# Kernel optimization log

Hardware: AMD Instinct MI355X
Metric: run time of the kernel (lower is better)

## Reference

```python
import math
import jax, jax.numpy as jnp
import numpy as np

H = 16          # n_heads
WIN = 512       # window_size (causal, one-sided)
BS = 64         # block_size


def setup_inputs() -> dict:
    key = jax.random.key(0)
    ks = jax.random.split(key, 5)
    B, T, D = 2, 4096, 1024
    x = jax.random.normal(ks[0], (B, T, D), dtype=jnp.float32)
    init = 0.02
    Wq = jax.random.normal(ks[1], (D, D), dtype=jnp.float32) * init
    Wk = jax.random.normal(ks[2], (D, D), dtype=jnp.float32) * init
    Wv = jax.random.normal(ks[3], (D, D), dtype=jnp.float32) * init
    Wo = jax.random.normal(ks[4], (D, D), dtype=jnp.float32) * init
    return {"x": x, "Wq": Wq, "Wk": Wk, "Wv": Wv, "Wo": Wo}


def _sliding_window_attn(q, k, v):
    """Causal sliding-window attention, banded/block-sparse form.

    q,k,v: (B, H, T, hd). Only key blocks within the window of each query
    block are gathered, honoring the sparsity the torch mask encodes.
    """
    B, Hn, T, hd = q.shape
    nb = T // BS                   # number of blocks
    nw1 = WIN // BS + 1            # key blocks touching a query block
    scale = 1.0 / math.sqrt(hd)

    qb = q.reshape(B, Hn, nb, BS, hd)
    kb = k.reshape(B, Hn, nb, BS, hd)
    vb = v.reshape(B, Hn, nb, BS, hd)

    offs = jnp.arange(-(WIN // BS), 1)                 # (nw1,)
    idx_raw = jnp.arange(nb)[:, None] + offs[None, :]  # (nb, nw1)
    idx = jnp.clip(idx_raw, 0, nb - 1)

    kg = jnp.take(kb, idx, axis=2)   # (B,H,nb,nw1,BS,hd)
    vg = jnp.take(vb, idx, axis=2)

    scores = jnp.einsum('bhnqd,bhnwkd->bhnqwk', qb, kg) * scale

    qpos = (jnp.arange(nb) * BS)[:, None, None, None] + jnp.arange(BS)[None, :, None, None]  # (nb,BS,1,1)
    kpos = (idx_raw * BS)[:, None, :, None] + jnp.arange(BS)[None, None, None, :]            # (nb,1,nw1,BS)
    valid = (idx_raw[:, None, :, None] >= 0) & (kpos <= qpos) & (qpos - kpos < WIN)
    scores = jnp.where(valid[None, None], scores, -1e9)

    p = jax.nn.softmax(scores.reshape(B, Hn, nb, BS, nw1 * BS), axis=-1)
    p = p.reshape(B, Hn, nb, BS, nw1, BS)
    out = jnp.einsum('bhnqwk,bhnwkd->bhnqd', p, vg)
    return out.reshape(B, Hn, T, hd)


def reference(x, Wq, Wk, Wv, Wo):
    B, T, D = x.shape
    hd = D // H

    def proj(W):  # torch Linear: x @ W.T
        return (x @ W.T).reshape(B, T, H, hd).transpose(0, 2, 1, 3)

    q, k, v = proj(Wq), proj(Wk), proj(Wv)
    out = _sliding_window_attn(q, k, v)            # (B,H,T,hd)
    out = out.transpose(0, 2, 1, 3).reshape(B, T, D)
    return out @ Wo.T
```

## Files before the change

### kernel.cpp

```cpp
#include <hip/hip_runtime.h>

#define DI static __device__ __forceinline__

typedef __attribute__((ext_vector_type(8))) short short8;
typedef __attribute__((ext_vector_type(4))) float f32x4;

DI unsigned short f2bf(float f) {
    union { float f; unsigned int u; } v; v.f = f;
    unsigned int r = v.u + 0x7FFFu + ((v.u >> 16) & 1u);
    return (unsigned short)(r >> 16);
}

DI unsigned int f2bf2(float lo, float hi) {
    return (unsigned int)f2bf(lo) | ((unsigned int)f2bf(hi) << 16);
}

DI void gload_lds16(const void* g, void* l) {
    __builtin_amdgcn_global_load_lds(
        (const __attribute__((address_space(1))) void*)g,
        (__attribute__((address_space(3))) void*)l, 16, 0, 0);
}

DI short8 ldsfrag(const void* base, int row, int bytecol) {
    return *(const short8*)((const char*)base + row * 128 + (bytecol ^ ((row & 7) << 4)));
}

__global__ __launch_bounds__(256) void k_cvt(
    const float* __restrict__ x, const float* __restrict__ wq,
    const float* __restrict__ wk, const float* __restrict__ wv,
    const float* __restrict__ wo,
    unsigned short* __restrict__ xb, unsigned short* __restrict__ wqb,
    unsigned short* __restrict__ wkb, unsigned short* __restrict__ wvb,
    unsigned short* __restrict__ wob)
{
    int idx = (blockIdx.x * 256 + threadIdx.x) * 8;
    const float* src; unsigned short* dst; int off;
    if (idx < 8388608) {
        src = x; dst = xb; off = idx;
    } else {
        int rel = idx - 8388608;
        int sel = rel >> 20;
        off = rel & 1048575;
        switch (sel) {
            case 0:  src = wq; dst = wqb; break;
            case 1:  src = wk; dst = wkb; break;
            case 2:  src = wv; dst = wvb; break;
            default: src = wo; dst = wob; break;
        }
    }
    float4 v0 = *(const float4*)(src + off);
    float4 v1 = *(const float4*)(src + off + 4);
    uint4 o;
    o.x = f2bf2(v0.x, v0.y);
    o.y = f2bf2(v0.z, v0.w);
    o.z = f2bf2(v1.x, v1.y);
    o.w = f2bf2(v1.z, v1.w);
    *(uint4*)(dst + off) = o;
}

DI void gemm_core(const unsigned short* __restrict__ Ag,
                  const unsigned short* __restrict__ Bg,
                  int m0, int n0, char* smem, f32x4 acc[4][4])
{
    const int t = threadIdx.x, lane = t & 63;
    const int wid = t >> 6, wr = wid >> 2, wc = wid & 3;
    const int kl = lane & 15, hi = lane >> 4;

#pragma unroll
    for (int m = 0; m < 4; ++m)
#pragma unroll
        for (int n = 0; n < 4; ++n)
            acc[m][n] = f32x4{0.f, 0.f, 0.f, 0.f};

    const int ca  = t,       ra  = ca  >> 2, sa  = ((ca  & 3) ^ ((ra  >> 1) & 3)) * 8;
    const int cb0 = t,       rb0 = cb0 >> 2, sb0 = ((cb0 & 3) ^ ((rb0 >> 1) & 3)) * 8;
    const int cb1 = t + 512, rb1 = cb1 >> 2, sb1 = ((cb1 & 3) ^ ((rb1 >> 1) & 3)) * 8;
    const unsigned short* pa  = Ag + (long)(m0 + ra)  * 1024 + sa;
    const unsigned short* pb0 = Bg + (long)(n0 + rb0) * 1024 + sb0;
    const unsigned short* pb1 = Bg + (long)(n0 + rb1) * 1024 + sb1;

#define STAGE(TILE, BUF) do {                                          \
        char* _sb = smem + (BUF) * 24576;                              \
        gload_lds16(pa  + (TILE) * 32, _sb + ca * 16);                 \
        gload_lds16(pb0 + (TILE) * 32, _sb + 8192 + cb0 * 16);         \
        gload_lds16(pb1 + (TILE) * 32, _sb + 8192 + cb1 * 16);         \
    } while (0)

    STAGE(0, 0);
    STAGE(1, 1);

    const int swz = ((hi ^ ((kl >> 1) & 3)) << 4);
    const int aoff = (wr * 64 + kl) * 64 + swz;
    const int boff = 8192 + (wc * 64 + kl) * 64 + swz;

#define KSTEP(KS, CUR, PRE, ISSUE, VM) do {                                   \
        asm volatile("s_waitcnt vmcnt(" VM ")" ::: "memory");                 \
        __builtin_amdgcn_s_barrier();                                         \
        __builtin_amdgcn_sched_barrier(0);                                    \
        if (ISSUE) STAGE((KS) + 2, PRE);                                      \
        const char* _ab = smem + (CUR) * 24576 + aoff;                        \
        const char* _bb = smem + (CUR) * 24576 + boff;                        \
        short8 _fa[4], _fb[4];                                                \
        _Pragma("unroll")                                                     \
        for (int m = 0; m < 4; ++m) _fa[m] = *(const short8*)(_ab + m * 1024);\
        _Pragma("unroll")                                                     \
        for (int n = 0; n < 4; ++n) _fb[n] = *(const short8*)(_bb + n * 1024);\
        __builtin_amdgcn_s_setprio(1);                                        \
        _Pragma("unroll")                                                     \
        for (int m = 0; m < 4; ++m)                                           \
        _Pragma("unroll")                                                     \
            for (int n = 0; n < 4; ++n)                                       \
                acc[m][n] = __builtin_amdgcn_mfma_f32_16x16x32_bf16(          \
                    _fa[m], _fb[n], acc[m][n], 0, 0, 0);                      \
        __builtin_amdgcn_s_setprio(0);                                        \
    } while (0)

    for (int u = 0; u < 10; ++u) {
        const int ks = u * 3;
        KSTEP(ks + 0, 0, 2, 1, "3");
        KSTEP(ks + 1, 1, 0, 1, "3");
        KSTEP(ks + 2, 2, 1, 1, "3");
    }
    KSTEP(30, 0, 2, 0, "3");
    KSTEP(31, 1, 0, 0, "0");
#undef KSTEP
#undef STAGE
}

DI void gemm_core128(const unsigned short* __restrict__ Ag,
                     const unsigned short* __restrict__ Bg,
                     int m0, int n0, char* smem, f32x4 acc[4][4])
{
    const int t = threadIdx.x, lane = t & 63;
    const int wid = t >> 6, wr = wid >> 1, wc = wid & 1;
    const int kl = lane & 15, hi = lane >> 4;

#pragma unroll
    for (int m = 0; m < 4; ++m)
#pragma unroll
        for (int n = 0; n < 4; ++n)
            acc[m][n] = f32x4{0.f, 0.f, 0.f, 0.f};

    const int ca0 = t,       ra0 = ca0 >> 2, sa0 = ((ca0 & 3) ^ ((ra0 >> 1) & 3)) * 8;
    const int ca1 = t + 256, ra1 = ca1 >> 2, sa1 = ((ca1 & 3) ^ ((ra1 >> 1) & 3)) * 8;
    const unsigned short* pa0 = Ag + (long)(m0 + ra0) * 1024 + sa0;
    const unsigned short* pa1 = Ag + (long)(m0 + ra1) * 1024 + sa1;
    const unsigned short* pb0 = Bg + (long)(n0 + ra0) * 1024 + sa0;
    const unsigned short* pb1 = Bg + (long)(n0 + ra1) * 1024 + sa1;

#define STAGE(TILE, BUF) do {                                          \
        char* _sb = smem + (BUF) * 16384;                              \
        gload_lds16(pa0 + (TILE) * 32, _sb + ca0 * 16);                \
        gload_lds16(pa1 + (TILE) * 32, _sb + ca1 * 16);                \
        gload_lds16(pb0 + (TILE) * 32, _sb + 8192 + ca0 * 16);         \
        gload_lds16(pb1 + (TILE) * 32, _sb + 8192 + ca1 * 16);         \
    } while (0)

    STAGE(0, 0);
    STAGE(1, 1);

    const int swz = ((hi ^ ((kl >> 1) & 3)) << 4);
    const int aoff = (wr * 64 + kl) * 64 + swz;
    const int boff = 8192 + (wc * 64 + kl) * 64 + swz;

#define KSTEP(KS, CUR, PRE, ISSUE, VM) do {                                   \
        asm volatile("s_waitcnt vmcnt(" VM ")" ::: "memory");                 \
        __builtin_amdgcn_s_barrier();                                         \
        __builtin_amdgcn_sched_barrier(0);                                    \
        if (ISSUE) STAGE((KS) + 2, PRE);                                      \
        const char* _ab = smem + (CUR) * 16384 + aoff;                        \
        const char* _bb = smem + (CUR) * 16384 + boff;                        \
        short8 _fa[4], _fb[4];                                                \
        _Pragma("unroll")                                                     \
        for (int m = 0; m < 4; ++m) _fa[m] = *(const short8*)(_ab + m * 1024);\
        _Pragma("unroll")                                                     \
        for (int n = 0; n < 4; ++n) _fb[n] = *(const short8*)(_bb + n * 1024);\
        __builtin_amdgcn_s_setprio(1);                                        \
        _Pragma("unroll")                                                     \
        for (int m = 0; m < 4; ++m)                                           \
        _Pragma("unroll")                                                     \
            for (int n = 0; n < 4; ++n)                                       \
                acc[m][n] = __builtin_amdgcn_mfma_f32_16x16x32_bf16(          \
                    _fa[m], _fb[n], acc[m][n], 0, 0, 0);                      \
        __builtin_amdgcn_s_setprio(0);                                        \
    } while (0)

    for (int u = 0; u < 10; ++u) {
        const int ks = u * 3;
        KSTEP(ks + 0, 0, 2, 1, "4");
        KSTEP(ks + 1, 1, 0, 1, "4");
        KSTEP(ks + 2, 2, 1, 1, "4");
    }
    KSTEP(30, 0, 2, 0, "4");
    KSTEP(31, 1, 0, 0, "0");
#undef KSTEP
#undef STAGE
}

__global__ __launch_bounds__(512, 4) void k_gemm_qkv(
    const unsigned short* __restrict__ xb,
    const unsigned short* __restrict__ wqb, const unsigned short* __restrict__ wkb,
    const unsigned short* __restrict__ wvb,
    unsigned short* __restrict__ Qo, unsigned short* __restrict__ Ko,
    unsigned short* __restrict__ VTo)
{
    extern __shared__ char smem[];
    const int bx = blockIdx.x, by = blockIdx.y;
    const int w = by >> 2, nb = by & 3;
    const unsigned short* Bw = (w == 0) ? wqb : ((w == 1) ? wkb : wvb);
    const float sc = (w == 0) ? 0.18033688011112042f : 1.0f;

    f32x4 acc[4][4];
    gemm_core(xb, Bw, bx * 128, nb * 256, smem, acc);

    const int t = threadIdx.x, lane = t & 63, wid = t >> 6;
    const int wr = wid >> 2, wc = wid & 3, kl = lane & 15, hi = lane >> 4;
    const int h = nb * 4 + wc;

    if (w < 2) {
        unsigned short* Ow = (w == 0) ? Qo : Ko;
#pragma unroll
        for (int m = 0; m < 4; ++m)
#pragma unroll
            for (int r = 0; r < 4; ++r) {
                int grow = bx * 128 + wr * 64 + m * 16 + hi * 4 + r;
                int bi = grow >> 12, tt = grow & 4095;
                unsigned short* rowp = Ow + ((long)(bi * 16 + h) * 4096 + tt) * 64;
#pragma unroll
                for (int n = 0; n < 4; ++n)
                    rowp[n * 16 + kl] = f2bf(acc[m][n][r] * sc);
            }
    } else {
#pragma unroll
        for (int m = 0; m < 4; ++m)
#pragma unroll
            for (int r = 0; r < 4; ++r) {
                int grow = bx * 128 + wr * 64 + m * 16 + hi * 4 + r;
                int bi = grow >> 12, tt = grow & 4095;
                unsigned short* hb = VTo + (long)(bi * 16 + h) * 262144;
#pragma unroll
                for (int n = 0; n < 4; ++n) {
                    int d = n * 16 + kl;
                    hb[(long)d * 4096 + tt] = f2bf(acc[m][n][r]);
                }
            }
    }
}

__global__ __launch_bounds__(512) void k_attn(
    const unsigned short* __restrict__ Q, const unsigned short* __restrict__ K,
    const unsigned short* __restrict__ VT, unsigned short* __restrict__ AO)
{
    __shared__ unsigned short Qs[8192];
    __shared__ unsigned short Ks[2][4096], Vs[2][4096];
    const int t = threadIdx.x, lane = t & 63, wid = t >> 6;
    const int kl = lane & 15, hi = lane >> 4;
    const int bid = blockIdx.x;
    const int sid = (bid & 7) * 128 + (bid >> 3);
    const int qi = sid & 31, bh = sid >> 5;
    const int b = bh >> 4, h = bh & 15;
    const int iA = qi * 2, iB = qi * 2 + 1;
    const int myI = (wid < 4) ? iA : iB;
    const char* qg = (const char*)(Q + ((long)bh * 4096 + qi * 128) * 64);
    const char* kg = (const char*)(K + (long)bh * 4096 * 64);
    const char* vg = (const char*)(VT + (long)bh * 64 * 4096);

    const int cq0 = t, cq1 = t + 512;
    const int rq0 = cq0 >> 3, sq0 = ((cq0 & 7) * 16) ^ ((rq0 & 7) << 4);
    const int rq1 = cq1 >> 3, sq1 = ((cq1 & 7) * 16) ^ ((rq1 & 7) << 4);
    const int rk = t >> 3, swk = ((t & 7) * 16) ^ ((rk & 7) << 4);
    const char* kgt = kg + rk * 128 + swk;
    const char* vgt = vg + rk * 8192 + swk;

    const int jlo = (iA >= 8) ? iA - 8 : 0;
    const int jhi = iB;

    gload_lds16(qg + rq0 * 128 + sq0, (char*)Qs + cq0 * 16);
    gload_lds16(qg + rq1 * 128 + sq1, (char*)Qs + cq1 * 16);
    gload_lds16(kgt + jlo * 8192, (char*)Ks[0] + t * 16);
    gload_lds16(vgt + jlo * 128,  (char*)Vs[0] + t * 16);
    __syncthreads();

    short8 aq[2];
    aq[0] = ldsfrag(Qs, wid * 16 + kl, hi * 16);
    aq[1] = ldsfrag(Qs, wid * 16 + kl, 64 + hi * 16);

    float lsum[4] = {0.f, 0.f, 0.f, 0.f};
    f32x4 o[4];
#pragma unroll
    for (int nt = 0; nt < 4; ++nt) o[nt] = f32x4{0.f, 0.f, 0.f, 0.f};

    const int qrow = (wid & 3) * 16 + hi * 4;
    char* pw = (char*)Qs + wid * 2048;

    for (int j = jlo; j <= jhi; ++j) {
        const int buf = (j - jlo) & 1;
        if (j < jhi) {
            const int nb = buf ^ 1;
            gload_lds16(kgt + (j + 1) * 8192, (char*)Ks[nb] + t * 16);
            gload_lds16(vgt + (j + 1) * 128,  (char*)Vs[nb] + t * 16);
        }

        const bool act = (wid < 4) ? (j <= iA) : (j >= iB - 8);
        if (act) {
            f32x4 s[4];
#pragma unroll
            for (int nt = 0; nt < 4; ++nt) {
                s[nt] = f32x4{0.f, 0.f, 0.f, 0.f};
#pragma unroll
                for (int kk = 0; kk < 2; ++kk)
                    s[nt] = __builtin_amdgcn_mfma_f32_16x16x32_bf16(
                        aq[kk], ldsfrag(Ks[buf], nt * 16 + kl, kk * 64 + hi * 16),
                        s[nt], 0, 0, 0);
            }

            if (j == myI) {
#pragma unroll
                for (int nt = 0; nt < 4; ++nt) {
                    int key = nt * 16 + kl;
#pragma unroll
                    for (int r = 0; r < 4; ++r)
                        if (key > qrow + r) s[nt][r] = -1e9f;
                }
            } else if (myI - j == 8) {
#pragma unroll
                for (int nt = 0; nt < 4; ++nt) {
                    int key = nt * 16 + kl;
#pragma unroll
                    for (int r = 0; r < 4; ++r)
                        if (key <= qrow + r) s[nt][r] = -1e9f;
                }
            }

#pragma unroll
            for (int nt = 0; nt < 4; ++nt)
#pragma unroll
                for (int r = 0; r < 4; ++r) {
                    float p = exp2f(s[nt][r]);
                    s[nt][r] = p;
                    lsum[r] += p;
                }

#pragma unroll
            for (int nt = 0; nt < 4; ++nt)
#pragma unroll
                for (int r = 0; r < 4; ++r) {
                    int q = hi * 4 + r;
                    int colb = (nt * 16 + kl) * 2;
                    *(unsigned short*)(pw + q * 128 + (colb ^ ((q & 7) << 4))) =
                        f2bf(s[nt][r]);
                }

            short8 pa0 = ldsfrag(pw, kl, hi * 16);
            short8 pa1 = ldsfrag(pw, kl, 64 + hi * 16);
#pragma unroll
            for (int nt = 0; nt < 4; ++nt) {
                o[nt] = __builtin_amdgcn_mfma_f32_16x16x32_bf16(
                    pa0, ldsfrag(Vs[buf], nt * 16 + kl, hi * 16), o[nt], 0, 0, 0);
                o[nt] = __builtin_amdgcn_mfma_f32_16x16x32_bf16(
                    pa1, ldsfrag(Vs[buf], nt * 16 + kl, 64 + hi * 16), o[nt], 0, 0, 0);
            }
        }

        __syncthreads();
    }

#pragma unroll
    for (int d = 1; d < 16; d <<= 1)
#pragma unroll
        for (int r = 0; r < 4; ++r) lsum[r] += __shfl_xor(lsum[r], d);

    float inv[4];
#pragma unroll
    for (int r = 0; r < 4; ++r) inv[r] = 1.0f / lsum[r];
#pragma unroll
    for (int r = 0; r < 4; ++r) {
        int tt = qi * 128 + wid * 16 + hi * 4 + r;
        unsigned short* rowp = AO + ((long)(b * 4096 + tt)) * 1024 + h * 64;
#pragma unroll
        for (int nt = 0; nt < 4; ++nt)
            rowp[nt * 16 + kl] = f2bf(o[nt][r] * inv[r]);
    }
}

__global__ __launch_bounds__(256, 3) void k_gemm_out(
    const unsigned short* __restrict__ AO, const unsigned short* __restrict__ wob,
    float* __restrict__ out)
{
    extern __shared__ char smem[];
    const int bx = blockIdx.x, nb = blockIdx.y;
    f32x4 acc[4][4];
    gemm_core128(AO, wob, bx * 128, nb * 128, smem, acc);

    const int t = threadIdx.x, lane = t & 63, wid = t >> 6;
    const int wr = wid >> 1, wc = wid & 1, kl = lane & 15, hi = lane >> 4;
#pragma unroll
    for (int m = 0; m < 4; ++m)
#pragma unroll
        for (int r = 0; r < 4; ++r) {
            int grow = bx * 128 + wr * 64 + m * 16 + hi * 4 + r;
            float* rowp = out + (long)grow * 1024 + nb * 128 + wc * 64;
#pragma unroll
            for (int n = 0; n < 4; ++n)
                rowp[n * 16 + kl] = acc[m][n][r];
        }
}

extern "C" void kernel_launch(void* const* d_in, const int* in_sizes, int n_in,
                              void* d_out, int out_size, void* d_ws, size_t ws_size,
                              hipStream_t stream) {
    const float* x  = (const float*)d_in[0];
    const float* wq = (const float*)d_in[1];
    const float* wk = (const float*)d_in[2];
    const float* wv = (const float*)d_in[3];
    const float* wo = (const float*)d_in[4];

    char* ws = (char*)d_ws;
    const size_t MB = 1024 * 1024;
    unsigned short* xb  = (unsigned short*)(ws);
    unsigned short* wqb = (unsigned short*)(ws + 16 * MB);
    unsigned short* wkb = (unsigned short*)(ws + 18 * MB);
    unsigned short* wvb = (unsigned short*)(ws + 20 * MB);
    unsigned short* wob = (unsigned short*)(ws + 22 * MB);
    unsigned short* Qp  = (unsigned short*)(ws + 24 * MB);
    unsigned short* Kp  = (unsigned short*)(ws + 40 * MB);
    unsigned short* VTp = (unsigned short*)(ws + 56 * MB);
    unsigned short* AOp = xb;

    hipFuncSetAttribute((const void*)k_gemm_qkv,
                        hipFuncAttributeMaxDynamicSharedMemorySize, 73728);
    hipFuncSetAttribute((const void*)k_gemm_out,
                        hipFuncAttributeMaxDynamicSharedMemorySize, 49152);

    dim3 blk(256);
    k_cvt<<<6144, blk, 0, stream>>>(x, wq, wk, wv, wo,
                                    xb, wqb, wkb, wvb, wob);
    k_gemm_qkv<<<dim3(64, 12), 512, 73728, stream>>>(xb, wqb, wkb, wvb,
                                                     Qp, Kp, VTp);
    k_attn<<<1024, 512, 0, stream>>>(Qp, Kp, VTp, AOp);
    k_gemm_out<<<dim3(64, 8), 256, 49152, stream>>>(AOp, wob, (float*)d_out);
}
```

Baseline: 135.6 us.

## Enlarge attention tile to 256 query rows, two sub-tiles per wave

Each attention block now covers four 64-row query blocks (256 rows) instead of two, and each wave handles 32 query rows as two 16-row sub-tiles. Every K/V block staged in LDS is therefore reused by more queries, so less K/V traffic and fewer synchronisations are needed per query. Q fragments are now loaded straight from global memory into registers instead of being staged through LDS. The trade-off is half as many workgroups (512), a longer serial key loop of up to 12 blocks, more accumulator registers per wave, and waves sitting idle at more iterations because of the window band.

```diff
diff --git a/kernel.cpp b/kernel.cpp
--- a/kernel.cpp
+++ b/kernel.cpp
@@ -251,47 +251,47 @@
     const unsigned short* __restrict__ Q, const unsigned short* __restrict__ K,
     const unsigned short* __restrict__ VT, unsigned short* __restrict__ AO)
 {
-    __shared__ unsigned short Qs[8192];
+    __shared__ unsigned short Ps[8192];
     __shared__ unsigned short Ks[2][4096], Vs[2][4096];
     const int t = threadIdx.x, lane = t & 63, wid = t >> 6;
     const int kl = lane & 15, hi = lane >> 4;
     const int bid = blockIdx.x;
-    const int sid = (bid & 7) * 128 + (bid >> 3);
-    const int qi = sid & 31, bh = sid >> 5;
+    const int sid = (bid & 7) * 64 + (bid >> 3);
+    const int qi = sid & 15, bh = sid >> 4;
     const int b = bh >> 4, h = bh & 15;
-    const int iA = qi * 2, iB = qi * 2 + 1;
-    const int myI = (wid < 4) ? iA : iB;
-    const char* qg = (const char*)(Q + ((long)bh * 4096 + qi * 128) * 64);
+    const int myI = qi * 4 + (wid >> 1);
+    const int rbase = (wid >> 1) * 64 + (wid & 1) * 32;
     const char* kg = (const char*)(K + (long)bh * 4096 * 64);
     const char* vg = (const char*)(VT + (long)bh * 64 * 4096);
 
-    const int cq0 = t, cq1 = t + 512;
-    const int rq0 = cq0 >> 3, sq0 = ((cq0 & 7) * 16) ^ ((rq0 & 7) << 4);
-    const int rq1 = cq1 >> 3, sq1 = ((cq1 & 7) * 16) ^ ((rq1 & 7) << 4);
+    short8 aq[2][2];
+#pragma unroll
+    for (int sub = 0; sub < 2; ++sub)
+#pragma unroll
+        for (int kk = 0; kk < 2; ++kk) {
+            long row = (long)bh * 4096 + qi * 256 + rbase + sub * 16 + kl;
+            aq[sub][kk] = *(const short8*)(Q + row * 64 + kk * 32 + hi * 8);
+        }
+
     const int rk = t >> 3, swk = ((t & 7) * 16) ^ ((rk & 7) << 4);
     const char* kgt = kg + rk * 128 + swk;
     const char* vgt = vg + rk * 8192 + swk;
 
-    const int jlo = (iA >= 8) ? iA - 8 : 0;
-    const int jhi = iB;
-
-    gload_lds16(qg + rq0 * 128 + sq0, (char*)Qs + cq0 * 16);
-    gload_lds16(qg + rq1 * 128 + sq1, (char*)Qs + cq1 * 16);
+    const int jlo = (qi * 4 >= 8) ? qi * 4 - 8 : 0;
+    const int jhi = qi * 4 + 3;
+
     gload_lds16(kgt + jlo * 8192, (char*)Ks[0] + t * 16);
     gload_lds16(vgt + jlo * 128,  (char*)Vs[0] + t * 16);
     __syncthreads();
 
-    short8 aq[2];
-    aq[0] = ldsfrag(Qs, wid * 16 + kl, hi * 16);
-    aq[1] = ldsfrag(Qs, wid * 16 + kl, 64 + hi * 16);
-
-    float lsum[4] = {0.f, 0.f, 0.f, 0.f};
-    f32x4 o[4];
-#pragma unroll
-    for (int nt = 0; nt < 4; ++nt) o[nt] = f32x4{0.f, 0.f, 0.f, 0.f};
-
-    const int qrow = (wid & 3) * 16 + hi * 4;
-    char* pw = (char*)Qs + wid * 2048;
+    float lsum[2][4] = {{0.f, 0.f, 0.f, 0.f}, {0.f, 0.f, 0.f, 0.f}};
+    f32x4 o[2][4];
+#pragma unroll
+    for (int sub = 0; sub < 2; ++sub)
+#pragma unroll
+        for (int nt = 0; nt < 4; ++nt) o[sub][nt] = f32x4{0.f, 0.f, 0.f, 0.f};
+
+    char* pw = (char*)Ps + wid * 2048;
 
     for (int j = jlo; j <= jhi; ++j) {
         const int buf = (j - jlo) & 1;
@@ -301,65 +301,72 @@
             gload_lds16(vgt + (j + 1) * 128,  (char*)Vs[nb] + t * 16);
         }
 
-        const bool act = (wid < 4) ? (j <= iA) : (j >= iB - 8);
+        const bool act = (j <= myI) && (j >= myI - 8);
         if (act) {
-            f32x4 s[4];
-#pragma unroll
-            for (int nt = 0; nt < 4; ++nt) {
-                s[nt] = f32x4{0.f, 0.f, 0.f, 0.f};
-#pragma unroll
-                for (int kk = 0; kk < 2; ++kk)
-                    s[nt] = __builtin_amdgcn_mfma_f32_16x16x32_bf16(
-                        aq[kk], ldsfrag(Ks[buf], nt * 16 + kl, kk * 64 + hi * 16),
-                        s[nt], 0, 0, 0);
-            }
-
-            if (j == myI) {
+#pragma unroll
+            for (int sub = 0; sub < 2; ++sub) {
+                const int qrow = (wid & 1) * 32 + sub * 16 + hi * 4;
+                f32x4 s[4];
 #pragma unroll
                 for (int nt = 0; nt < 4; ++nt) {
-                    int key = nt * 16 + kl;
-#pragma unroll
-                    for (int r = 0; r < 4; ++r)
-                        if (key > qrow + r) s[nt][r] = -1e9f;
+                    s[nt] = f32x4{0.f, 0.f, 0.f, 0.f};
+#pragma unroll
+                    for (int kk = 0; kk < 2; ++kk)
+                        s[nt] = __builtin_amdgcn_mfma_f32_16x16x32_bf16(
+                            aq[sub][kk],
+                            ldsfrag(Ks[buf], nt * 16 + kl, kk * 64 + hi * 16),
+                            s[nt], 0, 0, 0);
                 }
-            } else if (myI - j == 8) {
+
+                if (j == myI) {
+#pragma unroll
+                    for (int nt = 0; nt < 4; ++nt) {
+                        int key = nt * 16 + kl;
+#pragma unroll
+                        for (int r = 0; r < 4; ++r)
+                            if (key > qrow + r) s[nt][r] = -1e9f;
+                    }
+                } else if (myI - j == 8) {
+#pragma unroll
+                    for (int nt = 0; nt < 4; ++nt) {
+                        int key = nt * 16 + kl;
+#pragma unroll
+                        for (int r = 0; r < 4; ++r)
+                            if (key <= qrow + r) s[nt][r] = -1e9f;
+                    }
+                }
+
+#pragma unroll
+                for (int nt = 0; nt < 4; ++nt)
+#pragma unroll
+                    for (int r = 0; r < 4; ++r) {
+                        float p = exp2f(s[nt][r]);
+                        s[nt][r] = p;
+                        lsum[sub][r] += p;
+                    }
+
+#pragma unroll
+                for (int nt = 0; nt < 4; ++nt)
+#pragma unroll
+                    for (int r = 0; r < 4; ++r) {
+                        int q = hi * 4 + r;
+                        int colb = (nt * 16 + kl) * 2;
+                        *(unsigned short*)(pw + q * 128 +
+                            (colb ^ ((q & 7) << 4))) = f2bf(s[nt][r]);
+                    }
+
+                short8 pa0 = ldsfrag(pw, kl, hi * 16);
+                short8 pa1 = ldsfrag(pw, kl, 64 + hi * 16);
 #pragma unroll
                 for (int nt = 0; nt < 4; ++nt) {
-                    int key = nt * 16 + kl;
-#pragma unroll
-                    for (int r = 0; r < 4; ++r)
-                        if (key <= qrow + r) s[nt][r] = -1e9f;
+                    o[sub][nt] = __builtin_amdgcn_mfma_f32_16x16x32_bf16(
+                        pa0, ldsfrag(Vs[buf], nt * 16 + kl, hi * 16),
+                        o[sub][nt], 0, 0, 0);
+                    o[sub][nt] = __builtin_amdgcn_mfma_f32_16x16x32_bf16(
+                        pa1, ldsfrag(Vs[buf], nt * 16 + kl, 64 + hi * 16),
+                        o[sub][nt], 0, 0, 0);
                 }
             }
-
-#pragma unroll
-            for (int nt = 0; nt < 4; ++nt)
-#pragma unroll
-                for (int r = 0; r < 4; ++r) {
-                    float p = exp2f(s[nt][r]);
-                    s[nt][r] = p;
-                    lsum[r] += p;
-                }
-
-#pragma unroll
-            for (int nt = 0; nt < 4; ++nt)
-#pragma unroll
-                for (int r = 0; r < 4; ++r) {
-                    int q = hi * 4 + r;
-                    int colb = (nt * 16 + kl) * 2;
-                    *(unsigned short*)(pw + q * 128 + (colb ^ ((q & 7) << 4))) =
-                        f2bf(s[nt][r]);
-                }
-
-            short8 pa0 = ldsfrag(pw, kl, hi * 16);
-            short8 pa1 = ldsfrag(pw, kl, 64 + hi * 16);
-#pragma unroll
-            for (int nt = 0; nt < 4; ++nt) {
-                o[nt] = __builtin_amdgcn_mfma_f32_16x16x32_bf16(
-                    pa0, ldsfrag(Vs[buf], nt * 16 + kl, hi * 16), o[nt], 0, 0, 0);
-                o[nt] = __builtin_amdgcn_mfma_f32_16x16x32_bf16(
-                    pa1, ldsfrag(Vs[buf], nt * 16 + kl, 64 + hi * 16), o[nt], 0, 0, 0);
-            }
         }
 
         __syncthreads();
@@ -368,19 +375,23 @@
 #pragma unroll
     for (int d = 1; d < 16; d <<= 1)
 #pragma unroll
-        for (int r = 0; r < 4; ++r) lsum[r] += __shfl_xor(lsum[r], d);
-
-    float inv[4];
-#pragma unroll
-    for (int r = 0; r < 4; ++r) inv[r] = 1.0f / lsum[r];
-#pragma unroll
-    for (int r = 0; r < 4; ++r) {
-        int tt = qi * 128 + wid * 16 + hi * 4 + r;
-        unsigned short* rowp = AO + ((long)(b * 4096 + tt)) * 1024 + h * 64;
-#pragma unroll
-        for (int nt = 0; nt < 4; ++nt)
-            rowp[nt * 16 + kl] = f2bf(o[nt][r] * inv[r]);
-    }
+        for (int sub = 0; sub < 2; ++sub)
+#pragma unroll
+            for (int r = 0; r < 4; ++r)
+                lsum[sub][r] += __shfl_xor(lsum[sub][r], d);
+
+#pragma unroll
+    for (int sub = 0; sub < 2; ++sub)
+#pragma unroll
+        for (int r = 0; r < 4; ++r) {
+            float inv = 1.0f / lsum[sub][r];
+            int tt = qi * 256 + rbase + sub * 16 + hi * 4 + r;
+            unsigned short* rowp =
+                AO + ((long)(b * 4096 + tt)) * 1024 + h * 64;
+#pragma unroll
+            for (int nt = 0; nt < 4; ++nt)
+                rowp[nt * 16 + kl] = f2bf(o[sub][nt][r] * inv);
+        }
 }
 
 __global__ __launch_bounds__(256, 3) void k_gemm_out(
@@ -437,6 +448,6 @@
                                     xb, wqb, wkb, wvb, wob);
     k_gemm_qkv<<<dim3(64, 12), 512, 73728, stream>>>(xb, wqb, wkb, wvb,
                                                      Qp, Kp, VTp);
-    k_attn<<<1024, 512, 0, stream>>>(Qp, Kp, VTp, AOp);
+    k_attn<<<512, 512, 0, stream>>>(Qp, Kp, VTp, AOp);
     k_gemm_out<<<dim3(64, 8), 256, 49152, stream>>>(AOp, wob, (float*)d_out);
 }
```

After: 152.9 us. 12.8% more time.
